# Kernel tuning notes

Hardware: AMD Instinct MI355X
Metric: run time of the kernel (lower is better)

## Reference

```python
import jax, jax.numpy as jnp
import numpy as np


def conv3d(x, w, b):
    # x: [B,C,D,H,W], w: [O,I,3,3,3], padding=1, stride=1
    y = jax.lax.conv_general_dilated(
        x, w, window_strides=(1, 1, 1), padding=[(1, 1)] * 3,
        dimension_numbers=("NCDHW", "OIDHW", "NCDHW"))
    return y + b[None, :, None, None, None]


def trilinear_sample(x, cd, ch, cw):
    # x: [B,C,D,H,W]; cd/ch/cw: [B,K,D,H,W] float sampling coords.
    # Zero padding outside the volume (invalid corners masked to 0).
    B, C, D, H, W = x.shape
    d0 = jnp.floor(cd); h0 = jnp.floor(ch); w0 = jnp.floor(cw)
    fd, fh, fw = cd - d0, ch - h0, cw - w0
    d0 = d0.astype(jnp.int32); h0 = h0.astype(jnp.int32); w0 = w0.astype(jnp.int32)
    gather = jax.vmap(lambda xb, z, y, xx: xb[:, z, y, xx])  # -> [B,C,K,D,H,W]
    out = jnp.zeros((B, C) + cd.shape[1:], x.dtype)
    for dz in (0, 1):
        wz = fd if dz else 1.0 - fd
        zi = d0 + dz
        for dy in (0, 1):
            wy = fh if dy else 1.0 - fh
            yi = h0 + dy
            for dx in (0, 1):
                wx = fw if dx else 1.0 - fw
                xi = w0 + dx
                valid = ((zi >= 0) & (zi < D) & (yi >= 0) & (yi < H)
                         & (xi >= 0) & (xi < W)).astype(x.dtype)
                v = gather(x, jnp.clip(zi, 0, D - 1), jnp.clip(yi, 0, H - 1),
                           jnp.clip(xi, 0, W - 1))
                out = out + (wz * wy * wx * valid)[:, None] * v
    return out


def deform_conv3d(x, offsets, mask, w, b):
    # Modulated deformable 3D conv (DCNv2-style), kernel 3x3x3, pad 1, stride 1.
    # offsets: [B,81,D,H,W] = 27 taps x (dd,dh,dw); mask: [B,27,D,H,W].
    B, C, D, H, W = x.shape
    K = 27
    off = offsets.reshape(B, K, 3, D, H, W)
    kd, kh, kw = jnp.meshgrid(jnp.arange(3), jnp.arange(3), jnp.arange(3), indexing="ij")
    tap_d = (kd.reshape(-1) - 1).astype(x.dtype)[None, :, None, None, None]
    tap_h = (kh.reshape(-1) - 1).astype(x.dtype)[None, :, None, None, None]
    tap_w = (kw.reshape(-1) - 1).astype(x.dtype)[None, :, None, None, None]
    gd = jnp.arange(D, dtype=x.dtype)[None, None, :, None, None]
    gh = jnp.arange(H, dtype=x.dtype)[None, None, None, :, None]
    gw = jnp.arange(W, dtype=x.dtype)[None, None, None, None, :]
    cd = gd + tap_d + off[:, :, 0]
    ch = gh + tap_h + off[:, :, 1]
    cw = gw + tap_w + off[:, :, 2]
    sampled = trilinear_sample(x, cd, ch, cw) * mask[:, None]  # [B,C,K,D,H,W]
    out = jnp.einsum("bckdhw,ock->bodhw", sampled, w.reshape(w.shape[0], C, K))
    return out + b[None, :, None, None, None]


def mdconv3d(x, ow, ob, w, b):
    # MDConv3d: internal offset/mask predictor + modulated deformable conv.
    d = conv3d(x, ow, ob)
    offsets, mask = d[:, :81], jax.nn.sigmoid(d[:, 81:])
    return deform_conv3d(x, offsets, mask, w, b)


def forward(x, ow1, ob1, w1, b1, ow2, ob2, w2, b2, ow3, ob3, w3, b3,
            defo_w, defo_b, c3d_w, c3d_b):
    h = jax.nn.relu(mdconv3d(x, ow1, ob1, w1, b1))
    h = jax.nn.relu(mdconv3d(h, ow2, ob2, w2, b2))
    h = jax.nn.relu(mdconv3d(h, ow3, ob3, w3, b3))
    d = conv3d(h, defo_w, defo_b)
    offsets, alpha = d[:, :81], jax.nn.sigmoid(d[:, 81:])
    return deform_conv3d(x, offsets, alpha, c3d_w, c3d_b)


def setup_inputs() -> dict:
    key = jax.random.key(0)
    ks = jax.random.split(key, 16)
    B, C, D, H, W = 1, 256, 8, 32, 32
    M = 256  # mdim
    OFF_SCALE = 0.02  # small init so predicted offsets stay moderate

    def p(k, shape):
        return jax.random.normal(k, shape, jnp.float32) * OFF_SCALE

    inp = {"x": jax.random.normal(ks[0], (B, C, D, H, W), jnp.float32)}
    c_ins = [C, M, M]
    for i, cin in enumerate(c_ins, 1):
        inp[f"ow{i}"] = p(ks[2 * i - 1], (108, cin, 3, 3, 3))
        inp[f"ob{i}"] = jnp.zeros((108,), jnp.float32)
        inp[f"w{i}"] = p(ks[2 * i], (M, cin, 3, 3, 3))
        inp[f"b{i}"] = jnp.zeros((M,), jnp.float32)
    inp["defo_w"] = p(ks[13], (108, M, 3, 3, 3))
    inp["defo_b"] = jnp.zeros((108,), jnp.float32)
    inp["c3d_w"] = p(ks[14], (256, C, 3, 3, 3))
    inp["c3d_b"] = jnp.zeros((256,), jnp.float32)
    return inp


def reference(x, ow1, ob1, w1, b1, ow2, ob2, w2, b2, ow3, ob3, w3, b3,
              defo_w, defo_b, c3d_w, c3d_b):
    return forward(x, ow1, ob1, w1, b1, ow2, ob2, w2, b2, ow3, ob3, w3, b3,
                   defo_w, defo_b, c3d_w, c3d_b)
```

## Files before the change

### kernel.cpp

```cpp
#include <hip/hip_runtime.h>
#include <cstdint>

#define NPOS 8192
#define KTOT 6912
#define XP_ROWS 11560
#define XP_SY 34
#define XP_SZ 1156
#define KS 4
#define KSL 1728
#define NCHUNK 27

typedef float  facc_t __attribute__((ext_vector_type(4)));
typedef short  bf8_t  __attribute__((ext_vector_type(8)));
typedef unsigned short ub8_t __attribute__((ext_vector_type(8)));

__device__ __forceinline__ unsigned short f2bf(float f) {
    unsigned u = __float_as_uint(f);
    u = (u + 0x7FFFu + ((u >> 16) & 1u)) >> 16;
    return (unsigned short)u;
}
__device__ __forceinline__ float bf2f(unsigned short u) {
    return __uint_as_float(((unsigned)u) << 16);
}

#define GAS(p) ((const __attribute__((address_space(1))) void*)(p))
#define LAS(p) ((__attribute__((address_space(3))) void*)(p))

__global__ __launch_bounds__(256) void zero_k(unsigned short* __restrict__ dst) {
    ub8_t zz = {0,0,0,0,0,0,0,0};
    *(ub8_t*)&dst[((size_t)blockIdx.x * 256 + threadIdx.x) * 8] = zz;
}

__global__ __launch_bounds__(256) void pad_x_t(const float* __restrict__ x,
                                               unsigned short* __restrict__ XpA) {
    __shared__ unsigned short T[256 * 33];
    int b = blockIdx.x;
    int z = b >> 5, y = b & 31;
    int t = threadIdx.x;
    int c8 = t >> 5, xv = t & 31;
#pragma unroll 4
    for (int i = 0; i < 32; ++i) {
        int c = i * 8 + c8;
        T[c * 33 + xv] = f2bf(x[c * NPOS + (z << 10) + (y << 5) + xv]);
    }
    __syncthreads();
    int rowb = ((z + 1) * XP_SZ + (y + 1) * XP_SY + 1) * 256;
#pragma unroll 4
    for (int j = 0; j < 32; ++j) {
        XpA[rowb + j * 256 + t] = T[t * 33 + j];
    }
}

__global__ __launch_bounds__(256) void wtrans_all(
    const float* __restrict__ o1, const float* __restrict__ o2,
    const float* __restrict__ o3, const float* __restrict__ o4,
    const float* __restrict__ m1, const float* __restrict__ m2,
    const float* __restrict__ m3, const float* __restrict__ m4,
    unsigned short* __restrict__ wtoff, unsigned short* __restrict__ wtmain) {
    __shared__ float T[6912];
    int b = blockIdx.x, t = threadIdx.x;
    const float* src; unsigned short* dst; int o, O;
    if (b < 512) {
        int L = b >> 7; o = b & 127; O = 108;
        src = (L == 0) ? o1 : (L == 1) ? o2 : (L == 2) ? o3 : o4;
        dst = wtoff + ((size_t)(L * 128 + o)) * KTOT;
    } else {
        int b2 = b - 512;
        int L = b2 >> 8; o = b2 & 255; O = 256;
        src = (L == 0) ? m1 : (L == 1) ? m2 : (L == 2) ? m3 : m4;
        dst = wtmain + ((size_t)(L * 256 + o)) * KTOT;
    }
    if (o < O) {
#pragma unroll 3
        for (int i = 0; i < 27; ++i) T[i * 256 + t] = src[(size_t)o * KTOT + i * 256 + t];
        __syncthreads();
#pragma unroll 3
        for (int i = 0; i < 27; ++i) {
            int kc = i * 256 + t;
            int c = kc & 255, k = kc >> 8;
            dst[kc] = f2bf(T[c * 27 + k]);
        }
    } else {
#pragma unroll 3
        for (int i = 0; i < 27; ++i) dst[i * 256 + t] = 0;
    }
}

template<bool DEFORM>
__global__ __launch_bounds__(256, 2)
void fgemm(const unsigned short* __restrict__ Xp,
           const unsigned short* __restrict__ wt,
           const float* __restrict__ dbuf,
           float* __restrict__ parts) {
    constexpr int O   = DEFORM ? 256 : 128;
    constexpr int PWN = DEFORM ? 4 : 2;
    __shared__ unsigned short Bs[2][64 * 64] __attribute__((aligned(16)));

    const int t = threadIdx.x;
    const int wave = t >> 6, lane = t & 63;
    const int q = lane >> 4, r = lane & 15;
    const int pbase = blockIdx.x * 64;
    const int ks = blockIdx.y;
    const int kstart = ks * KSL;

    const int obw = DEFORM ? (wave * 64) : ((wave >> 1) * 64);
    const int pfb = DEFORM ? 0 : ((wave & 1) * 32);

    const int pl = t >> 2;
    const int csub = (t & 3) * 16;
    const int p = pbase + pl;
    const int z = p >> 10, y = (p >> 5) & 31, xx = p & 31;
    const int g0 = (t & 3) * 2;
    const int wr0 = pl * 64 + ((g0 ^ (pl & 7)) << 3);
    const int wr1 = pl * 64 + (((g0 + 1) ^ (pl & 7)) << 3);

    const int plc = (wave << 4) + (lane >> 3);
    const int cgrp = ((lane & 7) ^ (plc & 7)) << 3;
    const int pA = pbase + plc, pB = pA + 8;
    const int zA = pA >> 10, yA = (pA >> 5) & 31, xA = pA & 31;
    const int zB = pB >> 10, yB = (pB >> 5) & 31, xB = pB & 31;

    facc_t acc[4][PWN];
#pragma unroll
    for (int i = 0; i < 4; ++i)
#pragma unroll
        for (int ip = 0; ip < PWN; ++ip) acc[i][ip] = (facc_t){0.f, 0.f, 0.f, 0.f};

    float cw[8];
    int row0 = 0;
    int kprev = -1;

    for (int sc = 0; sc <= NCHUNK; ++sc) {
        const int haveS = (sc < NCHUNK);
        const int haveM = (sc > 0);

        bf8_t afr[2][4];
        if (haveM) {
            const int mkc0 = kstart + (sc - 1) * 64;
#pragma unroll
            for (int sl = 0; sl < 2; ++sl)
#pragma unroll
                for (int i = 0; i < 4; ++i)
                    afr[sl][i] = *(const bf8_t*)&wt[(size_t)(obw + i * 16 + r) * KTOT + mkc0 + sl * 32 + q * 8];
        }

        ub8_t st[16];
        if (haveS) {
            const int skc0 = kstart + sc * 64;
            const int sk = skc0 >> 8;
            const int sc0 = skc0 & 255;
            if constexpr (DEFORM) {
                if (sk != kprev) {
                    kprev = sk;
                    const int kd = sk / 9, kh = (sk / 3) % 3, kw = sk % 3;
                    float od  = dbuf[(3 * sk + 0) * NPOS + p];
                    float oh  = dbuf[(3 * sk + 1) * NPOS + p];
                    float ow_ = dbuf[(3 * sk + 2) * NPOS + p];
                    float m   = dbuf[(81 + sk) * NPOS + p];
                    float cd = (float)(z + kd - 1) + od;
                    float ch = (float)(y + kh - 1) + oh;
                    float cx = (float)(xx + kw - 1) + ow_;
                    float fdf = floorf(cd), fhf = floorf(ch), fwf = floorf(cx);
                    float fd = cd - fdf, fh = ch - fhf, fw = cx - fwf;
                    float wz0 = 1.f - fd, wz1 = fd;
                    float wy0 = 1.f - fh, wy1 = fh;
                    float wx0 = 1.f - fw, wx1 = fw;
                    int id, ih, iw;
                    if (fdf < -1.f || fdf >= 8.f)  { wz0 = 0.f; wz1 = 0.f; id = 0; } else id = (int)fdf;
                    if (fhf < -1.f || fhf >= 32.f) { wy0 = 0.f; wy1 = 0.f; ih = 0; } else ih = (int)fhf;
                    if (fwf < -1.f || fwf >= 32.f) { wx0 = 0.f; wx1 = 0.f; iw = 0; } else iw = (int)fwf;
                    wz0 *= m; wz1 *= m;
                    float w00 = wz0 * wy0, w01 = wz0 * wy1, w10 = wz1 * wy0, w11 = wz1 * wy1;
                    cw[0] = w00 * wx0; cw[1] = w00 * wx1;
                    cw[2] = w01 * wx0; cw[3] = w01 * wx1;
                    cw[4] = w10 * wx0; cw[5] = w10 * wx1;
                    cw[6] = w11 * wx0; cw[7] = w11 * wx1;
                    row0 = (id + 1) * XP_SZ + (ih + 1) * XP_SY + (iw + 1);
                }
                const unsigned short* cb = Xp + (size_t)row0 * 256 + sc0 + csub;
#pragma unroll
                for (int j = 0; j < 8; ++j) {
                    const int roff = ((j >> 2) & 1) * XP_SZ + ((j >> 1) & 1) * XP_SY + (j & 1);
                    st[2 * j]     = *(const ub8_t*)(cb + roff * 256);
                    st[2 * j + 1] = *(const ub8_t*)(cb + roff * 256 + 8);
                }
            } else {
                const int kd = sk / 9, kh = (sk / 3) % 3, kw = sk % 3;
                const int rowA = (zA + kd) * XP_SZ + (yA + kh) * XP_SY + (xA + kw);
                const int rowB = (zB + kd) * XP_SZ + (yB + kh) * XP_SY + (xB + kw);
                unsigned short* lb = &Bs[sc & 1][wave << 10];
                __builtin_amdgcn_global_load_lds(GAS(Xp + (size_t)rowA * 256 + sc0 + cgrp), LAS(lb),       16, 0, 0);
                __builtin_amdgcn_global_load_lds(GAS(Xp + (size_t)rowB * 256 + sc0 + cgrp), LAS(lb + 512), 16, 0, 0);
            }
        }

        if (haveM) {
            const unsigned short* Bc = Bs[(sc - 1) & 1];
#pragma unroll
            for (int sl = 0; sl < 2; ++sl) {
                bf8_t bfr[PWN];
#pragma unroll
                for (int ip = 0; ip < PWN; ++ip) {
                    int brow = pfb + ip * 16 + r;
                    bfr[ip] = *(const bf8_t*)&Bc[brow * 64 + (((sl * 4 + q) ^ (brow & 7)) << 3)];
                }
#pragma unroll
                for (int i = 0; i < 4; ++i)
#pragma unroll
                    for (int ip = 0; ip < PWN; ++ip)
                        acc[i][ip] = __builtin_amdgcn_mfma_f32_16x16x32_bf16(afr[sl][i], bfr[ip], acc[i][ip], 0, 0, 0);
            }
        }

        if constexpr (DEFORM) {
            if (haveS) {
                float av[16];
#pragma unroll
                for (int e = 0; e < 16; ++e) av[e] = 0.f;
#pragma unroll
                for (int j = 0; j < 8; ++j) {
#pragma unroll
                    for (int e = 0; e < 8; ++e) {
                        av[e]     += cw[j] * bf2f(st[2 * j][e]);
                        av[8 + e] += cw[j] * bf2f(st[2 * j + 1][e]);
                    }
                }
                ub8_t v0, v1;
#pragma unroll
                for (int e = 0; e < 8; ++e) { v0[e] = f2bf(av[e]); v1[e] = f2bf(av[8 + e]); }
                unsigned short* Bn = Bs[sc & 1];
                *(ub8_t*)&Bn[wr0] = v0;
                *(ub8_t*)&Bn[wr1] = v1;
            }
        }
        __syncthreads();
    }

    float* pp = parts + (size_t)ks * O * NPOS;
#pragma unroll
    for (int i = 0; i < 4; ++i)
#pragma unroll
        for (int ip = 0; ip < PWN; ++ip)
#pragma unroll
            for (int reg = 0; reg < 4; ++reg) {
                int o = obw + i * 16 + q * 4 + reg;
                int px = pbase + pfb + ip * 16 + r;
                pp[(size_t)o * NPOS + px] = acc[i][ip][reg];
            }
}

__global__ __launch_bounds__(256) void ccombine(const float* __restrict__ parts,
                                                const float* __restrict__ ob,
                                                float* __restrict__ dbuf) {
    int b = blockIdx.x;
    int o = b >> 3;
    int p4 = ((b & 7) * 256 + threadIdx.x) * 4;
    float s0 = 0, s1 = 0, s2 = 0, s3 = 0;
#pragma unroll
    for (int s = 0; s < KS; ++s) {
        const float4 v = *(const float4*)&parts[((size_t)(s * 128 + o)) * NPOS + p4];
        s0 += v.x; s1 += v.y; s2 += v.z; s3 += v.w;
    }
    float bv = ob[o];
    s0 += bv; s1 += bv; s2 += bv; s3 += bv;
    if (o >= 81) {
        s0 = 1.f / (1.f + __expf(-s0));
        s1 = 1.f / (1.f + __expf(-s1));
        s2 = 1.f / (1.f + __expf(-s2));
        s3 = 1.f / (1.f + __expf(-s3));
    }
    *(float4*)&dbuf[(size_t)o * NPOS + p4] = make_float4(s0, s1, s2, s3);
}

__global__ __launch_bounds__(256) void dcombine_h(const float* __restrict__ parts,
                                                  const float* __restrict__ bias,
                                                  unsigned short* __restrict__ XpB) {
    __shared__ unsigned short T[64 * 66];
    int p0 = blockIdx.x * 64, o0 = blockIdx.y * 64;
    int t = threadIdx.x;
    int pl = t & 63, og = t >> 6;
#pragma unroll 4
    for (int j = 0; j < 16; ++j) {
        int ol = og * 16 + j;
        float s = 0.f;
#pragma unroll
        for (int sp = 0; sp < KS; ++sp)
            s += parts[((size_t)(sp * 256 + o0 + ol)) * NPOS + p0 + pl];
        s += bias[o0 + ol];
        T[ol * 66 + pl] = f2bf(fmaxf(s, 0.f));
    }
    __syncthreads();
    int c = t & 63, pr = t >> 6;
#pragma unroll 4
    for (int j = 0; j < 16; ++j) {
        int pl2 = j * 4 + pr;
        int pg = p0 + pl2;
        int zz = pg >> 10, yy = (pg >> 5) & 31, xv = pg & 31;
        int row = (zz + 1) * XP_SZ + (yy + 1) * XP_SY + xv + 1;
        XpB[(size_t)row * 256 + o0 + c] = T[c * 66 + pl2];
    }
}

__global__ __launch_bounds__(256) void dcombine_out(const float* __restrict__ parts,
                                                    const float* __restrict__ bias,
                                                    float* __restrict__ out) {
    int b = blockIdx.x;
    int o = b >> 3;
    int p4 = ((b & 7) * 256 + threadIdx.x) * 4;
    float s0 = 0, s1 = 0, s2 = 0, s3 = 0;
#pragma unroll
    for (int s = 0; s < KS; ++s) {
        const float4 v = *(const float4*)&parts[((size_t)(s * 256 + o)) * NPOS + p4];
        s0 += v.x; s1 += v.y; s2 += v.z; s3 += v.w;
    }
    float bv = bias[o];
    *(float4*)&out[(size_t)o * NPOS + p4] = make_float4(s0 + bv, s1 + bv, s2 + bv, s3 + bv);
}

extern "C" void kernel_launch(void* const* d_in, const int* in_sizes, int n_in,
                              void* d_out, int out_size, void* d_ws, size_t ws_size,
                              hipStream_t stream) {
    const float* x      = (const float*)d_in[0];
    const float* ow1    = (const float*)d_in[1];
    const float* ob1    = (const float*)d_in[2];
    const float* w1     = (const float*)d_in[3];
    const float* b1     = (const float*)d_in[4];
    const float* ow2    = (const float*)d_in[5];
    const float* ob2    = (const float*)d_in[6];
    const float* w2     = (const float*)d_in[7];
    const float* b2     = (const float*)d_in[8];
    const float* ow3    = (const float*)d_in[9];
    const float* ob3    = (const float*)d_in[10];
    const float* w3     = (const float*)d_in[11];
    const float* b3     = (const float*)d_in[12];
    const float* defo_w = (const float*)d_in[13];
    const float* defo_b = (const float*)d_in[14];
    const float* c3d_w  = (const float*)d_in[15];
    const float* c3d_b  = (const float*)d_in[16];
    float* out = (float*)d_out;

    unsigned short* XpA    = (unsigned short*)d_ws;
    unsigned short* XpB    = XpA + (size_t)XP_ROWS * 256;
    unsigned short* wtoff  = XpB + (size_t)XP_ROWS * 256;
    unsigned short* wtmain = wtoff + (size_t)4 * 128 * KTOT;
    float* dbufp = (float*)(wtmain + (size_t)4 * 256 * KTOT);
    float* parts = dbufp + (size_t)108 * NPOS;

    const dim3 blk(256);
    const dim3 gG(128, KS);

    zero_k<<<2890, blk, 0, stream>>>(XpA);
    pad_x_t<<<256, blk, 0, stream>>>(x, XpA);
    wtrans_all<<<1536, blk, 0, stream>>>(ow1, ow2, ow3, defo_w, w1, w2, w3, c3d_w, wtoff, wtmain);

    const float* cbias[4] = {ob1, ob2, ob3, defo_b};
    const float* dbias[4] = {b1, b2, b3, c3d_b};

    for (int L = 0; L < 4; ++L) {
        const unsigned short* featConv = (L == 0) ? XpA : XpB;
        const unsigned short* featDef  = (L == 3) ? XpA : featConv;
        fgemm<false><<<gG, blk, 0, stream>>>(featConv, wtoff + (size_t)L * 128 * KTOT, nullptr, parts);
        ccombine<<<864, blk, 0, stream>>>(parts, cbias[L], dbufp);
        fgemm<true><<<gG, blk, 0, stream>>>(featDef, wtmain + (size_t)L * 256 * KTOT, dbufp, parts);
        if (L < 3) dcombine_h<<<dim3(128, 4), blk, 0, stream>>>(parts, dbias[L], XpB);
        else       dcombine_out<<<2048, blk, 0, stream>>>(parts, dbias[L], out);
    }
}
```

Measured before the change: 795.3 us.

## Halve GEMM position tile to 32 and raise occupancy with packed bilinear math

Each fgemm block now covers 32 positions instead of 64, so the grid doubles and each wave owns a slice of output channels across all 32 positions. Each thread samples 8 channels instead of 16. The launch bound rises to 4 blocks per CU, and the trilinear accumulation uses packed float2 arithmetic with inline bf16 unpacking. The goal is more occupancy and parallelism to hide the latency of the gather and the loads. The cost is that weight fragments are reloaded per 32 positions, which doubles weight traffic per output, and registers are squeezed.

```diff
diff --git a/kernel.cpp b/kernel.cpp
--- a/kernel.cpp
+++ b/kernel.cpp
@@ -11,6 +11,7 @@
 #define NCHUNK 27
 
 typedef float  facc_t __attribute__((ext_vector_type(4)));
+typedef float  f2_t   __attribute__((ext_vector_type(2)));
 typedef short  bf8_t  __attribute__((ext_vector_type(8)));
 typedef unsigned short ub8_t __attribute__((ext_vector_type(8)));
 
@@ -18,9 +19,6 @@
     unsigned u = __float_as_uint(f);
     u = (u + 0x7FFFu + ((u >> 16) & 1u)) >> 16;
     return (unsigned short)u;
-}
-__device__ __forceinline__ float bf2f(unsigned short u) {
-    return __uint_as_float(((unsigned)u) << 16);
 }
 
 #define GAS(p) ((const __attribute__((address_space(1))) void*)(p))
@@ -87,44 +85,39 @@
 }
 
 template<bool DEFORM>
-__global__ __launch_bounds__(256, 2)
+__global__ __launch_bounds__(256, 4)
 void fgemm(const unsigned short* __restrict__ Xp,
            const unsigned short* __restrict__ wt,
            const float* __restrict__ dbuf,
            float* __restrict__ parts) {
-    constexpr int O   = DEFORM ? 256 : 128;
-    constexpr int PWN = DEFORM ? 4 : 2;
-    __shared__ unsigned short Bs[2][64 * 64] __attribute__((aligned(16)));
+    constexpr int O  = DEFORM ? 256 : 128;
+    constexpr int IO = DEFORM ? 4 : 2;
+    __shared__ unsigned short Bs[2][32 * 64] __attribute__((aligned(16)));
 
     const int t = threadIdx.x;
     const int wave = t >> 6, lane = t & 63;
     const int q = lane >> 4, r = lane & 15;
-    const int pbase = blockIdx.x * 64;
+    const int pbase = blockIdx.x * 32;
     const int ks = blockIdx.y;
     const int kstart = ks * KSL;
-
-    const int obw = DEFORM ? (wave * 64) : ((wave >> 1) * 64);
-    const int pfb = DEFORM ? 0 : ((wave & 1) * 32);
-
-    const int pl = t >> 2;
-    const int csub = (t & 3) * 16;
+    const int obw = wave * (O / 4);
+
+    const int pl = t >> 3;
+    const int csub = (t & 7) * 8;
     const int p = pbase + pl;
     const int z = p >> 10, y = (p >> 5) & 31, xx = p & 31;
-    const int g0 = (t & 3) * 2;
-    const int wr0 = pl * 64 + ((g0 ^ (pl & 7)) << 3);
-    const int wr1 = pl * 64 + (((g0 + 1) ^ (pl & 7)) << 3);
-
-    const int plc = (wave << 4) + (lane >> 3);
+    const int wrD = pl * 64 + (((t & 7) ^ (pl & 7)) << 3);
+
+    const int plc = (wave << 3) + (lane >> 3);
     const int cgrp = ((lane & 7) ^ (plc & 7)) << 3;
-    const int pA = pbase + plc, pB = pA + 8;
-    const int zA = pA >> 10, yA = (pA >> 5) & 31, xA = pA & 31;
-    const int zB = pB >> 10, yB = (pB >> 5) & 31, xB = pB & 31;
-
-    facc_t acc[4][PWN];
-#pragma unroll
-    for (int i = 0; i < 4; ++i)
-#pragma unroll
-        for (int ip = 0; ip < PWN; ++ip) acc[i][ip] = (facc_t){0.f, 0.f, 0.f, 0.f};
+    const int pC = pbase + plc;
+    const int zC = pC >> 10, yC = (pC >> 5) & 31, xC = pC & 31;
+
+    facc_t acc[IO][2];
+#pragma unroll
+    for (int i = 0; i < IO; ++i)
+#pragma unroll
+        for (int ip = 0; ip < 2; ++ip) acc[i][ip] = (facc_t){0.f, 0.f, 0.f, 0.f};
 
     float cw[8];
     int row0 = 0;
@@ -134,17 +127,17 @@
         const int haveS = (sc < NCHUNK);
         const int haveM = (sc > 0);
 
-        bf8_t afr[2][4];
+        bf8_t afr[2][IO];
         if (haveM) {
             const int mkc0 = kstart + (sc - 1) * 64;
 #pragma unroll
             for (int sl = 0; sl < 2; ++sl)
 #pragma unroll
-                for (int i = 0; i < 4; ++i)
+                for (int i = 0; i < IO; ++i)
                     afr[sl][i] = *(const bf8_t*)&wt[(size_t)(obw + i * 16 + r) * KTOT + mkc0 + sl * 32 + q * 8];
         }
 
-        ub8_t st[16];
+        ub8_t st[8];
         if (haveS) {
             const int skc0 = kstart + sc * 64;
             const int sk = skc0 >> 8;
@@ -181,16 +174,13 @@
 #pragma unroll
                 for (int j = 0; j < 8; ++j) {
                     const int roff = ((j >> 2) & 1) * XP_SZ + ((j >> 1) & 1) * XP_SY + (j & 1);
-                    st[2 * j]     = *(const ub8_t*)(cb + roff * 256);
-                    st[2 * j + 1] = *(const ub8_t*)(cb + roff * 256 + 8);
+                    st[j] = *(const ub8_t*)(cb + roff * 256);
                 }
             } else {
                 const int kd = sk / 9, kh = (sk / 3) % 3, kw = sk % 3;
-                const int rowA = (zA + kd) * XP_SZ + (yA + kh) * XP_SY + (xA + kw);
-                const int rowB = (zB + kd) * XP_SZ + (yB + kh) * XP_SY + (xB + kw);
-                unsigned short* lb = &Bs[sc & 1][wave << 10];
-                __builtin_amdgcn_global_load_lds(GAS(Xp + (size_t)rowA * 256 + sc0 + cgrp), LAS(lb),       16, 0, 0);
-                __builtin_amdgcn_global_load_lds(GAS(Xp + (size_t)rowB * 256 + sc0 + cgrp), LAS(lb + 512), 16, 0, 0);
+                const int rowC = (zC + kd) * XP_SZ + (yC + kh) * XP_SY + (xC + kw);
+                unsigned short* lb = &Bs[sc & 1][wave << 9];
+                __builtin_amdgcn_global_load_lds(GAS(Xp + (size_t)rowC * 256 + sc0 + cgrp), LAS(lb), 16, 0, 0);
             }
         }
 
@@ -198,39 +188,43 @@
             const unsigned short* Bc = Bs[(sc - 1) & 1];
 #pragma unroll
             for (int sl = 0; sl < 2; ++sl) {
-                bf8_t bfr[PWN];
-#pragma unroll
-                for (int ip = 0; ip < PWN; ++ip) {
-                    int brow = pfb + ip * 16 + r;
+                bf8_t bfr[2];
+#pragma unroll
+                for (int ip = 0; ip < 2; ++ip) {
+                    int brow = ip * 16 + r;
                     bfr[ip] = *(const bf8_t*)&Bc[brow * 64 + (((sl * 4 + q) ^ (brow & 7)) << 3)];
                 }
 #pragma unroll
-                for (int i = 0; i < 4; ++i)
-#pragma unroll
-                    for (int ip = 0; ip < PWN; ++ip)
+                for (int i = 0; i < IO; ++i)
+#pragma unroll
+                    for (int ip = 0; ip < 2; ++ip)
                         acc[i][ip] = __builtin_amdgcn_mfma_f32_16x16x32_bf16(afr[sl][i], bfr[ip], acc[i][ip], 0, 0, 0);
             }
         }
 
         if constexpr (DEFORM) {
             if (haveS) {
-                float av[16];
-#pragma unroll
-                for (int e = 0; e < 16; ++e) av[e] = 0.f;
+                f2_t av2[4];
+#pragma unroll
+                for (int e = 0; e < 4; ++e) av2[e] = (f2_t){0.f, 0.f};
 #pragma unroll
                 for (int j = 0; j < 8; ++j) {
-#pragma unroll
-                    for (int e = 0; e < 8; ++e) {
-                        av[e]     += cw[j] * bf2f(st[2 * j][e]);
-                        av[8 + e] += cw[j] * bf2f(st[2 * j + 1][e]);
+                    const unsigned* dw = (const unsigned*)&st[j];
+                    f2_t cwj = {cw[j], cw[j]};
+#pragma unroll
+                    for (int e = 0; e < 4; ++e) {
+                        unsigned d = dw[e];
+                        f2_t v = { __uint_as_float(d << 16), __uint_as_float(d & 0xffff0000u) };
+                        av2[e] += cwj * v;
                     }
                 }
-                ub8_t v0, v1;
-#pragma unroll
-                for (int e = 0; e < 8; ++e) { v0[e] = f2bf(av[e]); v1[e] = f2bf(av[8 + e]); }
-                unsigned short* Bn = Bs[sc & 1];
-                *(ub8_t*)&Bn[wr0] = v0;
-                *(ub8_t*)&Bn[wr1] = v1;
+                ub8_t v0;
+#pragma unroll
+                for (int e = 0; e < 4; ++e) {
+                    v0[2 * e]     = f2bf(av2[e][0]);
+                    v0[2 * e + 1] = f2bf(av2[e][1]);
+                }
+                *(ub8_t*)&Bs[sc & 1][wrD] = v0;
             }
         }
         __syncthreads();
@@ -238,13 +232,13 @@
 
     float* pp = parts + (size_t)ks * O * NPOS;
 #pragma unroll
-    for (int i = 0; i < 4; ++i)
-#pragma unroll
-        for (int ip = 0; ip < PWN; ++ip)
+    for (int i = 0; i < IO; ++i)
+#pragma unroll
+        for (int ip = 0; ip < 2; ++ip)
 #pragma unroll
             for (int reg = 0; reg < 4; ++reg) {
                 int o = obw + i * 16 + q * 4 + reg;
-                int px = pbase + pfb + ip * 16 + r;
+                int px = pbase + ip * 16 + r;
                 pp[(size_t)o * NPOS + px] = acc[i][ip][reg];
             }
 }
@@ -347,7 +341,7 @@
     float* parts = dbufp + (size_t)108 * NPOS;
 
     const dim3 blk(256);
-    const dim3 gG(128, KS);
+    const dim3 gG(256, KS);
 
     zero_k<<<2890, blk, 0, stream>>>(XpA);
     pad_x_t<<<256, blk, 0, stream>>>(x, XpA);
```

Measured after the change: 930.1 us. 16.9% more time.
